# Kernel optimization log

Measured on AMD Instinct MI355X. Metric: run time of the kernel, lower is better.

Reference implementation:

```python
import jax, jax.numpy as jnp
import numpy as np

N = 20000        # nodes
E = 320000       # edges (avg degree 16)
G = 128          # graphs in batch
D_IN = 128
H = 128          # hidden_dim
HEADS = 8
OUT = 2
BN_EPS = 1e-5


def _segment_softmax(logits, seg, num_segments):
    # numerically stable softmax over segments along leading dim
    m = jax.ops.segment_max(logits, seg, num_segments)
    e = jnp.exp(logits - m[seg])
    s = jax.ops.segment_sum(e, seg, num_segments)
    return e / (s[seg] + 1e-16)


def _forward(x, gin1_w1, gin1_b1, gin1_w2, gin1_b2,
             gin2_w1, gin2_b1, gin2_w2, gin2_b2,
             gin3_w1, gin3_b1, gin3_w2, gin3_b2,
             gin4_w1, gin4_b1, gin4_w2, gin4_b2,
             bn1_g, bn1_b, bn2_g, bn2_b, bn3_g, bn3_b, bn4_g, bn4_b, bn5_g, bn5_b,
             gat_w, gat_asrc, gat_adst, gat_bias,
             gate_w, gate_b, fc1_w, fc1_b, fc2_w, fc2_b,
             edge_index, batch):
    src, dst = edge_index[0], edge_index[1]

    def gin(h, w1, b1, w2, b2):
        # GINConv, eps=0: mlp(x + sum_{j->i} x_j)
        agg = jax.ops.segment_sum(h[src], dst, N)
        z = agg + h
        return jax.nn.relu(z @ w1 + b1) @ w2 + b2

    def bn(h, g, b):
        # BatchNorm1d with batch statistics (training-mode normalization)
        mu = h.mean(0)
        var = ((h - mu) ** 2).mean(0)
        return g * (h - mu) * jax.lax.rsqrt(var + BN_EPS) + b

    # dropout is identity at inference
    h = jax.nn.relu(bn(gin(x, gin1_w1, gin1_b1, gin1_w2, gin1_b2), bn1_g, bn1_b))
    h = jax.nn.relu(bn(gin(h, gin2_w1, gin2_b1, gin2_w2, gin2_b2), bn2_g, bn2_b))
    h = jax.nn.relu(bn(gin(h, gin3_w1, gin3_b1, gin3_w2, gin3_b2), bn3_g, bn3_b))
    h = jax.nn.relu(bn(gin(h, gin4_w1, gin4_b1, gin4_w2, gin4_b2), bn4_g, bn4_b))

    # GATConv(2H -> H, heads=HEADS, concat=False) with self-loops (PyG default)
    loop = jnp.arange(N)
    s = jnp.concatenate([src, loop])
    d = jnp.concatenate([dst, loop])
    xh = (h @ gat_w).reshape(N, HEADS, H)                     # [N, heads, H]
    a_s = jnp.einsum('nhc,hc->nh', xh, gat_asrc)              # [N, heads]
    a_d = jnp.einsum('nhc,hc->nh', xh, gat_adst)
    e = jax.nn.leaky_relu(a_s[s] + a_d[d], 0.2)               # [E+N, heads]
    alpha = _segment_softmax(e, d, N)                         # softmax over in-edges of dst
    out = jax.ops.segment_sum(alpha[:, :, None] * xh[s], d, N)  # [N, heads, H]
    h = out.mean(1) + gat_bias                                # concat=False -> mean heads
    h = jax.nn.relu(bn(h, bn5_g, bn5_b))

    # GlobalAttention pooling: softmax(gate_nn(x)) per graph, weighted sum
    gate_logit = (h @ gate_w + gate_b)[:, 0]                  # [N]
    gate = _segment_softmax(gate_logit, batch, G)
    pooled = jax.ops.segment_sum(gate[:, None] * h, batch, G)  # [G, H]

    return jax.nn.relu(pooled @ fc1_w + fc1_b) @ fc2_w + fc2_b  # [G, OUT]


def setup_inputs() -> dict:
    key = jax.random.key(0)
    kit = iter(jax.random.split(key, 64))

    def nrm(shape, s=0.05):
        return jax.random.normal(next(kit), shape, jnp.float32) * s

    inp = {}
    inp['x'] = jax.random.normal(next(kit), (N, D_IN), jnp.float32)
    inp['edge_index'] = jax.random.randint(next(kit), (2, E), 0, N)
    inp['batch'] = jnp.sort(jax.random.randint(next(kit), (N,), 0, G))
    gin_dims = [(D_IN, H), (H, 2 * H), (2 * H, 4 * H), (4 * H, 2 * H)]
    for i, (a, b) in enumerate(gin_dims, 1):
        inp[f'gin{i}_w1'] = nrm((a, b))
        inp[f'gin{i}_b1'] = jnp.zeros((b,), jnp.float32)
        inp[f'gin{i}_w2'] = nrm((b, b))
        inp[f'gin{i}_b2'] = jnp.zeros((b,), jnp.float32)
    for i, dd in enumerate([H, 2 * H, 4 * H, 2 * H, H], 1):
        inp[f'bn{i}_g'] = jnp.ones((dd,), jnp.float32)
        inp[f'bn{i}_b'] = jnp.zeros((dd,), jnp.float32)
    inp['gat_w'] = nrm((2 * H, HEADS * H))
    inp['gat_asrc'] = nrm((HEADS, H))
    inp['gat_adst'] = nrm((HEADS, H))
    inp['gat_bias'] = jnp.zeros((H,), jnp.float32)
    inp['gate_w'] = nrm((H, 1))
    inp['gate_b'] = jnp.zeros((1,), jnp.float32)
    inp['fc1_w'] = nrm((H, 128))
    inp['fc1_b'] = jnp.zeros((128,), jnp.float32)
    inp['fc2_w'] = nrm((128, OUT))
    inp['fc2_b'] = jnp.zeros((OUT,), jnp.float32)
    return inp


def reference(x, edge_index, batch,
              gin1_w1, gin1_b1, gin1_w2, gin1_b2,
              gin2_w1, gin2_b1, gin2_w2, gin2_b2,
              gin3_w1, gin3_b1, gin3_w2, gin3_b2,
              gin4_w1, gin4_b1, gin4_w2, gin4_b2,
              bn1_g, bn1_b, bn2_g, bn2_b, bn3_g, bn3_b, bn4_g, bn4_b, bn5_g, bn5_b,
              gat_w, gat_asrc, gat_adst, gat_bias,
              gate_w, gate_b, fc1_w, fc1_b, fc2_w, fc2_b):
    return _forward(x, gin1_w1, gin1_b1, gin1_w2, gin1_b2,
                    gin2_w1, gin2_b1, gin2_w2, gin2_b2,
                    gin3_w1, gin3_b1, gin3_w2, gin3_b2,
                    gin4_w1, gin4_b1, gin4_w2, gin4_b2,
                    bn1_g, bn1_b, bn2_g, bn2_b, bn3_g, bn3_b, bn4_g, bn4_b, bn5_g, bn5_b,
                    gat_w, gat_asrc, gat_adst, gat_bias,
                    gate_w, gate_b, fc1_w, fc1_b, fc2_w, fc2_b,
                    edge_index, batch)
```

## Files before the change

kernel.cpp:

```cpp
#include <hip/hip_runtime.h>
#include <hip/hip_bf16.h>
#include <math.h>

#define NN 20000
#define NE 320000
#define NG 128

using bf16x8 = __attribute__((ext_vector_type(8))) short;
using f32x4  = __attribute__((ext_vector_type(4))) float;

static __device__ __forceinline__ float lrelu(float v){ return v > 0.f ? v : 0.2f*v; }
static __device__ __forceinline__ float b2f(unsigned short u){ unsigned int v = ((unsigned int)u) << 16; return __uint_as_float(v); }
static __device__ __forceinline__ unsigned short f2b(float f){
  unsigned int x = __float_as_uint(f);
  unsigned int r = x + 0x7fffu + ((x >> 16) & 1u);
  return (unsigned short)(r >> 16);
}
static __device__ __forceinline__ void gl16(const unsigned short* g, unsigned short* l){
  __builtin_amdgcn_global_load_lds((const __attribute__((address_space(1))) void*)g,
                                   (__attribute__((address_space(3))) void*)l, 16, 0, 0);
}
static __device__ __forceinline__ uint4 bn8(uint4 u, const float* scs, const float* shs, int f0){
  float v[8] = { b2f(u.x & 0xffff), b2f(u.x >> 16), b2f(u.y & 0xffff), b2f(u.y >> 16),
                 b2f(u.z & 0xffff), b2f(u.z >> 16), b2f(u.w & 0xffff), b2f(u.w >> 16) };
  #pragma unroll
  for (int j = 0; j < 8; j++) v[j] = fmaxf(v[j]*scs[f0 + j] + shs[f0 + j], 0.f);
  uint4 p;
  p.x = (unsigned int)f2b(v[0]) | ((unsigned int)f2b(v[1]) << 16);
  p.y = (unsigned int)f2b(v[2]) | ((unsigned int)f2b(v[3]) << 16);
  p.z = (unsigned int)f2b(v[4]) | ((unsigned int)f2b(v[5]) << 16);
  p.w = (unsigned int)f2b(v[6]) | ((unsigned int)f2b(v[7]) << 16);
  return p;
}

__global__ void k_hist2(const int* __restrict__ dst, const int* __restrict__ batch,
                        int* __restrict__ deg, int* __restrict__ gdeg){
  int i = blockIdx.x*blockDim.x + threadIdx.x;
  if (i < NE) atomicAdd(&deg[dst[i]], 1);
  else if (i < NE + NN) atomicAdd(&gdeg[batch[i - NE]], 1);
}

__global__ void k_scan2(const int* __restrict__ deg, int* __restrict__ rowptr,
                        const int* __restrict__ gdeg, int* __restrict__ gptr){
  __shared__ int tmp[1024];
  int t = threadIdx.x;
  if (blockIdx.x == 0){
    const int CH = 20;
    int lo = t*CH, hi = min(lo + CH, NN);
    int loc[CH];
    int s = 0;
    for (int i = lo; i < hi; i++){ loc[i - lo] = deg[i]; s += loc[i - lo]; }
    tmp[t] = s; __syncthreads();
    for (int off = 1; off < 1024; off <<= 1){
      int u = (t >= off) ? tmp[t - off] : 0;
      __syncthreads();
      tmp[t] += u;
      __syncthreads();
    }
    int r = tmp[t] - s;
    if (t == 0) rowptr[0] = 0;
    for (int i = lo; i < hi; i++){ r += loc[i - lo]; rowptr[i + 1] = r; }
  } else {
    int v = (t < NG) ? gdeg[t] : 0;
    tmp[t] = v; __syncthreads();
    for (int off = 1; off < 1024; off <<= 1){
      int u = (t >= off) ? tmp[t - off] : 0;
      __syncthreads();
      tmp[t] += u;
      __syncthreads();
    }
    if (t == 0) gptr[0] = 0;
    if (t < NG) gptr[t + 1] = tmp[t];
  }
}

__global__ void k_fill(const int* __restrict__ src, const int* __restrict__ dst,
                       const int* __restrict__ ptr, int* __restrict__ cnt,
                       int* __restrict__ csrc){
  int e = blockIdx.x*blockDim.x + threadIdx.x;
  if (e < NE){
    int d = dst[e];
    int p = atomicAdd(&cnt[d], 1);
    csrc[ptr[d] + p] = src[e];
  }
}

struct WPrep {
  const float* W[9];
  unsigned short* Wt[9];
  int K[9];
  int Nn[9];
  int tileStart[10];
  const float* x;
  unsigned int* xb;
};

__global__ __launch_bounds__(256)
void k_prep2(WPrep P){
  __shared__ float tile[64][65];
  int b = blockIdx.x;
  if (b < P.tileStart[9]){
    int i = 0;
    while (i < 8 && b >= P.tileStart[i+1]) i++;
    int ti = b - P.tileStart[i];
    int K = P.K[i], Nn = P.Nn[i];
    int ntc = Nn >> 6;
    int k0 = (ti / ntc) << 6, n0 = (ti % ntc) << 6;
    int c = threadIdx.x & 63, ro = threadIdx.x >> 6;
    const float* W = P.W[i];
    #pragma unroll
    for (int rr = 0; rr < 16; rr++){
      int r = rr*4 + ro;
      tile[c][r] = W[(size_t)(k0 + r)*Nn + n0 + c];
    }
    __syncthreads();
    unsigned short* Wt = P.Wt[i];
    if (i == 8){
      int hh = n0 >> 7, cl0 = n0 & 127;
      #pragma unroll
      for (int cc = 0; cc < 16; cc++){
        int cidx = cc*4 + ro;
        Wt[(size_t)(cl0 + cidx)*2048 + hh*256 + k0 + c] = f2b(tile[cidx][c]*0.125f);
      }
    } else {
      #pragma unroll
      for (int cc = 0; cc < 16; cc++){
        int cidx = cc*4 + ro;
        Wt[(size_t)(n0 + cidx)*K + k0 + c] = f2b(tile[cidx][c]);
      }
    }
  } else {
    int idx = (b - P.tileStart[9])*256 + threadIdx.x;
    if (idx < NN*64){
      unsigned int lo = f2b(P.x[2*idx]);
      unsigned int hi = f2b(P.x[2*idx + 1]);
      P.xb[idx] = lo | (hi << 16);
    }
  }
}

__global__ void k_wasd(const float* __restrict__ W, const float* __restrict__ asrc,
                       const float* __restrict__ adst, unsigned short* __restrict__ Bt_sc){
  __shared__ float av[128];
  int b = blockIdx.x;
  int h = b & 7, isd = b >> 3;
  int k = threadIdx.x;
  if (k < 128) av[k] = (isd ? adst : asrc)[h*128 + k];
  __syncthreads();
  const float* Wr = W + (size_t)k*1024 + h*128;
  float s = 0.f;
  #pragma unroll 8
  for (int c = 0; c < 128; c++) s += Wr[c]*av[c];
  Bt_sc[b*256 + k] = f2b(s);
}

template<int MODE, int DU>
__global__ __launch_bounds__(256)
void k_agg(const unsigned int* __restrict__ hU, const int* __restrict__ ptr,
           const int* __restrict__ csrc, unsigned int* __restrict__ z,
           const double* __restrict__ stats, const float* __restrict__ g,
           const float* __restrict__ bb, const float* __restrict__ bias){
  const int d = DU*2;
  __shared__ float scs[MODE == 1 ? 512 : 1];
  __shared__ float shs[MODE == 1 ? 512 : 1];
  int t = threadIdx.x;
  if (MODE == 1){
    for (int f = t; f < d; f += 256){
      double inv = 1.0 / (double)NN;
      double mu  = stats[f]*inv;
      double var = stats[d + f]*inv - mu*mu;
      if (var < 0.0) var = 0.0;
      float sc = g[f] * rsqrtf((float)var + 1e-5f);
      scs[f] = sc;
      shs[f] = bb[f] - (float)mu*sc;
    }
    __syncthreads();
  }
  const int npb = 256/DU;
  int n  = blockIdx.x*npb + t/DU;
  int tl = t & (DU - 1);
  int f0 = 2*tl, f1 = f0 + 1;
  float sc0 = 0.f, sh0 = 0.f, sc1 = 0.f, sh1 = 0.f;
  if (MODE == 1){ sc0 = scs[f0]; sh0 = shs[f0]; sc1 = scs[f1]; sh1 = shs[f1]; }
  int beg = ptr[n], deg = ptr[n+1] - beg;
  unsigned int self = hU[(size_t)n*DU + tl];
  float a0, a1;
  if (MODE == 1){
    a0 = fmaxf(b2f(self & 0xffff)*sc0 + sh0, 0.f);
    a1 = fmaxf(b2f(self >> 16)   *sc1 + sh1, 0.f);
  } else {
    a0 = b2f(self & 0xffff);
    a1 = b2f(self >> 16);
  }
  int i = 0;
  for (; i + 8 <= deg; i += 8){
    unsigned int v[8];
    #pragma unroll
    for (int u = 0; u < 8; u++) v[u] = hU[(size_t)csrc[beg + i + u]*DU + tl];
    #pragma unroll
    for (int u = 0; u < 8; u++){
      if (MODE == 1){
        a0 += fmaxf(b2f(v[u] & 0xffff)*sc0 + sh0, 0.f);
        a1 += fmaxf(b2f(v[u] >> 16)   *sc1 + sh1, 0.f);
      } else {
        a0 += b2f(v[u] & 0xffff);
        a1 += b2f(v[u] >> 16);
      }
    }
  }
  for (; i < deg; i++){
    unsigned int v = hU[(size_t)csrc[beg + i]*DU + tl];
    if (MODE == 1){
      a0 += fmaxf(b2f(v & 0xffff)*sc0 + sh0, 0.f);
      a1 += fmaxf(b2f(v >> 16)   *sc1 + sh1, 0.f);
    } else {
      a0 += b2f(v & 0xffff);
      a1 += b2f(v >> 16);
    }
  }
  if (MODE == 2){
    a0 = fmaxf(a0 + bias[f0], 0.f);
    a1 = fmaxf(a1 + bias[f1], 0.f);
  }
  z[(size_t)n*DU + tl] = (unsigned int)f2b(a0) | ((unsigned int)f2b(a1) << 16);
}

template<int ACT, int OBF, int STATS, int PK, int BNA>
__global__ __launch_bounds__(256)
void k_gemm_mfma(const unsigned short* __restrict__ A, const unsigned short* __restrict__ Bt,
                 const float* __restrict__ bias, float* __restrict__ C,
                 unsigned short* __restrict__ Cb, double* __restrict__ stats,
                 const double* __restrict__ bnst, const float* __restrict__ bng,
                 const float* __restrict__ bnb,
                 int M, int Nn, int K){
  const int LDA = BNA ? 40 : 32;
  __shared__ unsigned short As[2][128*(BNA ? 40 : 32)];
  __shared__ unsigned short Bs[2][128*32];
  __shared__ float scs[BNA ? 512 : 1];
  __shared__ float shs[BNA ? 512 : 1];
  const int bm = blockIdx.y*128, bn = blockIdx.x*128;
  const int tid = threadIdx.x;
  const int lane = tid & 63;
  const int wave = tid >> 6;
  const int wm = (wave >> 1)*64, wn = (wave & 1)*64;
  const int lr = lane & 15, lq = lane >> 4;

  f32x4 acc[4][4];
  #pragma unroll
  for (int i = 0; i < 4; i++)
    #pragma unroll
    for (int j = 0; j < 4; j++) acc[i][j] = (f32x4){0.f,0.f,0.f,0.f};

  const int rowA = tid >> 2, q = tid & 3;
  const int ldsOff = wave*16*32;
  const int gmA0 = min(bm + rowA,      M-1);
  const int gmA1 = min(bm + rowA + 64, M-1);
  const unsigned short* pA0 = &A[(size_t)gmA0*K + q*8];
  const unsigned short* pA1 = &A[(size_t)gmA1*K + q*8];
  const unsigned short* pB0 = &Bt[(size_t)(bn + rowA)*K + q*8];
  const unsigned short* pB1 = &Bt[(size_t)(bn + rowA + 64)*K + q*8];

  if (BNA){
    for (int f = tid; f < K; f += 256){
      double inv = 1.0 / (double)NN;
      double mu  = bnst[f]*inv;
      double var = bnst[K + f]*inv - mu*mu;
      if (var < 0.0) var = 0.0;
      float sc = bng[f] * rsqrtf((float)var + 1e-5f);
      scs[f] = sc;
      shs[f] = bnb[f] - (float)mu*sc;
    }
    __syncthreads();
  }

  if (BNA){
    uint4 u0 = *(const uint4*)pA0;
    uint4 u1 = *(const uint4*)pA1;
    int f0 = q*8;
    *(uint4*)&As[0][ rowA      *LDA + q*8] = bn8(u0, scs, shs, f0);
    *(uint4*)&As[0][(rowA + 64)*LDA + q*8] = bn8(u1, scs, shs, f0);
  } else {
    gl16(pA0, &As[0][ldsOff]);
    gl16(pA1, &As[0][ldsOff] + 64*32);
  }
  gl16(pB0, &Bs[0][ldsOff]);
  gl16(pB1, &Bs[0][ldsOff] + 64*32);
  __syncthreads();

  int cur = 0;
  for (int k0 = 0; k0 < K; k0 += 32){
    const int kn = k0 + 32;
    uint4 nu0, nu1;
    if (kn < K){
      if (BNA){
        nu0 = *(const uint4*)(pA0 + kn);
        nu1 = *(const uint4*)(pA1 + kn);
      } else {
        gl16(pA0 + kn, &As[cur^1][ldsOff]);
        gl16(pA1 + kn, &As[cur^1][ldsOff] + 64*32);
      }
      gl16(pB0 + kn, &Bs[cur^1][ldsOff]);
      gl16(pB1 + kn, &Bs[cur^1][ldsOff] + 64*32);
    }
    bf16x8 af[4], bf[4];
    #pragma unroll
    for (int mi = 0; mi < 4; mi++)
      af[mi] = *(const bf16x8*)&As[cur][(wm + mi*16 + lr)*LDA + lq*8];
    #pragma unroll
    for (int ni = 0; ni < 4; ni++)
      bf[ni] = *(const bf16x8*)&Bs[cur][(wn + ni*16 + lr)*32 + lq*8];
    #pragma unroll
    for (int mi = 0; mi < 4; mi++)
      #pragma unroll
      for (int ni = 0; ni < 4; ni++)
        acc[mi][ni] = __builtin_amdgcn_mfma_f32_16x16x32_bf16(af[mi], bf[ni], acc[mi][ni], 0, 0, 0);
    if (BNA && kn < K){
      int f0 = kn + q*8;
      *(uint4*)&As[cur^1][ rowA      *LDA + q*8] = bn8(nu0, scs, shs, f0);
      *(uint4*)&As[cur^1][(rowA + 64)*LDA + q*8] = bn8(nu1, scs, shs, f0);
    }
    __syncthreads();
    cur ^= 1;
  }

  float cs[4] = {0.f,0.f,0.f,0.f}, cq[4] = {0.f,0.f,0.f,0.f};
  #pragma unroll
  for (int mi = 0; mi < 4; mi++){
    #pragma unroll
    for (int j = 0; j < 4; j++){
      int gm = bm + wm + mi*16 + lq*4 + j;
      if (gm < M){
        #pragma unroll
        for (int ni = 0; ni < 4; ni++){
          int gn = bn + wn + ni*16 + lr;
          float v = acc[mi][ni][j] + (bias ? bias[gn] : 0.f);
          if (ACT) v = fmaxf(v, 0.f);
          if (PK){ if (gn < 16) C[(size_t)gm*16 + gn] = v; }
          else if (OBF) Cb[(size_t)gm*Nn + gn] = f2b(v);
          else     C [(size_t)gm*Nn + gn] = v;
          if (STATS){ cs[ni] += v; cq[ni] += v*v; }
        }
      }
    }
  }
  if (STATS){
    #pragma unroll
    for (int ni = 0; ni < 4; ni++){
      float s = cs[ni], qq = cq[ni];
      s += __shfl_xor(s, 16); s += __shfl_xor(s, 32);
      qq += __shfl_xor(qq, 16); qq += __shfl_xor(qq, 32);
      if (lane < 16){
        int gn = bn + wn + ni*16 + lr;
        atomicAdd(&stats[gn],      (double)s);
        atomicAdd(&stats[Nn + gn], (double)qq);
      }
    }
  }
}

__global__ __launch_bounds__(256)
void k_gin1_mlp(const unsigned short* __restrict__ Z, const unsigned short* __restrict__ W1t,
                const float* __restrict__ b1, const unsigned short* __restrict__ W2t,
                const float* __restrict__ b2, unsigned short* __restrict__ Out,
                double* __restrict__ stats, int M){
  __shared__ unsigned short As[2][128*32];
  __shared__ unsigned short Bs[2][128*32];
  __shared__ unsigned short hid[128*136];
  const int bm = blockIdx.x*128;
  const int tid = threadIdx.x;
  const int lane = tid & 63;
  const int wave = tid >> 6;
  const int wm = (wave >> 1)*64, wn = (wave & 1)*64;
  const int lr = lane & 15, lq = lane >> 4;
  const int rowA = tid >> 2, q = tid & 3;
  const int ldsOff = wave*16*32;
  const int gm0 = min(bm + rowA,      M-1);
  const int gm1 = min(bm + rowA + 64, M-1);
  const unsigned short* pA0 = &Z[(size_t)gm0*128 + q*8];
  const unsigned short* pA1 = &Z[(size_t)gm1*128 + q*8];
  const unsigned short* pB0 = &W1t[(size_t)rowA*128 + q*8];
  const unsigned short* pB1 = &W1t[(size_t)(rowA + 64)*128 + q*8];

  f32x4 acc[4][4];
  #pragma unroll
  for (int i = 0; i < 4; i++)
    #pragma unroll
    for (int j = 0; j < 4; j++) acc[i][j] = (f32x4){0.f,0.f,0.f,0.f};

  gl16(pA0, &As[0][ldsOff]);
  gl16(pA1, &As[0][ldsOff] + 64*32);
  gl16(pB0, &Bs[0][ldsOff]);
  gl16(pB1, &Bs[0][ldsOff] + 64*32);
  __syncthreads();
  int cur = 0;
  for (int k0 = 0; k0 < 128; k0 += 32){
    int kn = k0 + 32;
    if (kn < 128){
      gl16(pA0 + kn, &As[cur^1][ldsOff]);
      gl16(pA1 + kn, &As[cur^1][ldsOff] + 64*32);
      gl16(pB0 + kn, &Bs[cur^1][ldsOff]);
      gl16(pB1 + kn, &Bs[cur^1][ldsOff] + 64*32);
    }
    bf16x8 af[4], bf[4];
    #pragma unroll
    for (int mi = 0; mi < 4; mi++)
      af[mi] = *(const bf16x8*)&As[cur][(wm + mi*16 + lr)*32 + lq*8];
    #pragma unroll
    for (int ni = 0; ni < 4; ni++)
      bf[ni] = *(const bf16x8*)&Bs[cur][(wn + ni*16 + lr)*32 + lq*8];
    #pragma unroll
    for (int mi = 0; mi < 4; mi++)
      #pragma unroll
      for (int ni = 0; ni < 4; ni++)
        acc[mi][ni] = __builtin_amdgcn_mfma_f32_16x16x32_bf16(af[mi], bf[ni], acc[mi][ni], 0, 0, 0);
    __syncthreads();
    cur ^= 1;
  }
  {
    float bv[4];
    #pragma unroll
    for (int ni = 0; ni < 4; ni++) bv[ni] = b1[wn + ni*16 + lr];
    #pragma unroll
    for (int mi = 0; mi < 4; mi++)
      #pragma unroll
      for (int j = 0; j < 4; j++){
        int row = wm + mi*16 + lq*4 + j;
        #pragma unroll
        for (int ni = 0; ni < 4; ni++){
          int col = wn + ni*16 + lr;
          hid[row*136 + col] = f2b(fmaxf(acc[mi][ni][j] + bv[ni], 0.f));
        }
      }
  }
  __syncthreads();

  f32x4 acc2[4][4];
  #pragma unroll
  for (int i = 0; i < 4; i++)
    #pragma unroll
    for (int j = 0; j < 4; j++) acc2[i][j] = (f32x4){0.f,0.f,0.f,0.f};
  const unsigned short* pC0 = &W2t[(size_t)rowA*128 + q*8];
  const unsigned short* pC1 = &W2t[(size_t)(rowA + 64)*128 + q*8];
  gl16(pC0, &Bs[0][ldsOff]);
  gl16(pC1, &Bs[0][ldsOff] + 64*32);
  __syncthreads();
  cur = 0;
  for (int k0 = 0; k0 < 128; k0 += 32){
    int kn = k0 + 32;
    if (kn < 128){
      gl16(pC0 + kn, &Bs[cur^1][ldsOff]);
      gl16(pC1 + kn, &Bs[cur^1][ldsOff] + 64*32);
    }
    bf16x8 af[4], bf[4];
    #pragma unroll
    for (int mi = 0; mi < 4; mi++)
      af[mi] = *(const bf16x8*)&hid[(wm + mi*16 + lr)*136 + k0 + lq*8];
    #pragma unroll
    for (int ni = 0; ni < 4; ni++)
      bf[ni] = *(const bf16x8*)&Bs[cur][(wn + ni*16 + lr)*32 + lq*8];
    #pragma unroll
    for (int mi = 0; mi < 4; mi++)
      #pragma unroll
      for (int ni = 0; ni < 4; ni++)
        acc2[mi][ni] = __builtin_amdgcn_mfma_f32_16x16x32_bf16(af[mi], bf[ni], acc2[mi][ni], 0, 0, 0);
    __syncthreads();
    cur ^= 1;
  }
  float cs[4] = {0.f,0.f,0.f,0.f}, cq[4] = {0.f,0.f,0.f,0.f};
  #pragma unroll
  for (int mi = 0; mi < 4; mi++){
    #pragma unroll
    for (int j = 0; j < 4; j++){
      int gm = bm + wm + mi*16 + lq*4 + j;
      if (gm < M){
        #pragma unroll
        for (int ni = 0; ni < 4; ni++){
          int gn = wn + ni*16 + lr;
          float v = acc2[mi][ni][j] + b2[gn];
          Out[(size_t)gm*128 + gn] = f2b(v);
          cs[ni] += v; cq[ni] += v*v;
        }
      }
    }
  }
  #pragma unroll
  for (int ni = 0; ni < 4; ni++){
    float s = cs[ni], qq = cq[ni];
    s += __shfl_xor(s, 16); s += __shfl_xor(s, 32);
    qq += __shfl_xor(qq, 16); qq += __shfl_xor(qq, 32);
    if (lane < 16){
      int gn = wn + ni*16 + lr;
      atomicAdd(&stats[gn],       (double)s);
      atomicAdd(&stats[128 + gn], (double)qq);
    }
  }
}

__global__ __launch_bounds__(256)
void k_gat_agg(const unsigned int* __restrict__ hU, const float* __restrict__ a_sd,
               const int* __restrict__ ptr, const int* __restrict__ csrc,
               const double* __restrict__ st, const float* __restrict__ g,
               const float* __restrict__ bb, unsigned int* __restrict__ agg){
  int n = blockIdx.x, t = threadIdx.x;
  __shared__ float scs[256], shs[256];
  __shared__ float elv[256][9];
  __shared__ int esrc[256];
  __shared__ float red[256];
  __shared__ float ms[8], ssinv[8], adn[8];
  __shared__ float partial[2][8][260];
  {
    int f = t;
    double inv = 1.0/(double)NN;
    double mu = st[f]*inv;
    double var = st[256 + f]*inv - mu*mu;
    if (var < 0.0) var = 0.0;
    float sc = g[f]*rsqrtf((float)var + 1e-5f);
    scs[f] = sc; shs[f] = bb[f] - (float)mu*sc;
  }
  if (t < 8) adn[t] = a_sd[n*16 + 8 + t];
  __syncthreads();
  int beg = ptr[n], deg = ptr[n+1] - beg, tot = deg + 1;
  int head = t >> 5, slot = t & 31;
  int grp = t >> 7, l = t & 127;
  float sc0 = scs[2*l], sh0 = shs[2*l], sc1 = scs[2*l+1], sh1 = shs[2*l+1];
  float acc[16];
  #pragma unroll
  for (int j = 0; j < 16; j++) acc[j] = 0.f;

  if (tot <= 256){
    for (int i = t; i < tot; i += 256) esrc[i] = (i < deg) ? csrc[beg + i] : n;
    __syncthreads();
    for (int i = t; i < tot*8; i += 256){
      int le = i >> 3, hh = i & 7;
      elv[le][hh] = lrelu(a_sd[esrc[le]*16 + hh] + adn[hh]);
    }
    __syncthreads();
    float mx = -1e30f;
    for (int e = slot; e < tot; e += 32) mx = fmaxf(mx, elv[e][head]);
    red[t] = mx; __syncthreads();
    #pragma unroll
    for (int off = 16; off >= 1; off >>= 1){
      if (slot < off) red[t] = fmaxf(red[t], red[t + off]);
      __syncthreads();
    }
    if (slot == 0) ms[head] = red[t];
    __syncthreads();
    float sm = 0.f;
    for (int e = slot; e < tot; e += 32){
      float ex = __expf(elv[e][head] - ms[head]);
      elv[e][head] = ex;
      sm += ex;
    }
    red[t] = sm; __syncthreads();
    #pragma unroll
    for (int off = 16; off >= 1; off >>= 1){
      if (slot < off) red[t] += red[t + off];
      __syncthreads();
    }
    if (slot == 0) ssinv[head] = 1.f / (red[t] + 1e-16f);
    __syncthreads();
    for (int e = grp; e < tot; e += 2){
      unsigned int u = hU[(size_t)esrc[e]*128 + l];
      float v0 = fmaxf(b2f(u & 0xffff)*sc0 + sh0, 0.f);
      float v1 = fmaxf(b2f(u >> 16)   *sc1 + sh1, 0.f);
      #pragma unroll
      for (int h = 0; h < 8; h++){
        float a = elv[e][h];
        acc[2*h]   += a*v0;
        acc[2*h+1] += a*v1;
      }
    }
    __syncthreads();
  } else {
    float mx = -1e30f;
    for (int e = slot; e < tot; e += 32){
      int s = (e < deg) ? csrc[beg + e] : n;
      mx = fmaxf(mx, lrelu(a_sd[s*16 + head] + adn[head]));
    }
    red[t] = mx; __syncthreads();
    #pragma unroll
    for (int off = 16; off >= 1; off >>= 1){
      if (slot < off) red[t] = fmaxf(red[t], red[t + off]);
      __syncthreads();
    }
    if (slot == 0) ms[head] = red[t];
    __syncthreads();
    float sm = 0.f;
    for (int e = slot; e < tot; e += 32){
      int s = (e < deg) ? csrc[beg + e] : n;
      sm += __expf(lrelu(a_sd[s*16 + head] + adn[head]) - ms[head]);
    }
    red[t] = sm; __syncthreads();
    #pragma unroll
    for (int off = 16; off >= 1; off >>= 1){
      if (slot < off) red[t] += red[t + off];
      __syncthreads();
    }
    if (slot == 0) ssinv[head] = 1.f / (red[t] + 1e-16f);
    __syncthreads();
    for (int c0 = 0; c0 < tot; c0 += 256){
      int ce = min(256, tot - c0);
      for (int i = t; i < ce*8; i += 256){
        int le = i >> 3, hh = i & 7;
        int s = (c0 + le < deg) ? csrc[beg + c0 + le] : n;
        if (hh == 0) esrc[le] = s;
        elv[le][hh] = __expf(lrelu(a_sd[s*16 + hh] + adn[hh]) - ms[hh]);
      }
      __syncthreads();
      for (int e = grp; e < ce; e += 2){
        unsigned int u = hU[(size_t)esrc[e]*128 + l];
        float v0 = fmaxf(b2f(u & 0xffff)*sc0 + sh0, 0.f);
        float v1 = fmaxf(b2f(u >> 16)   *sc1 + sh1, 0.f);
        #pragma unroll
        for (int h = 0; h < 8; h++){
          float a = elv[e][h];
          acc[2*h]   += a*v0;
          acc[2*h+1] += a*v1;
        }
      }
      __syncthreads();
    }
  }

  #pragma unroll
  for (int h = 0; h < 8; h++){
    partial[grp][h][2*l]   = acc[2*h];
    partial[grp][h][2*l+1] = acc[2*h+1];
  }
  __syncthreads();
  for (int o = t; o < 1024; o += 256){
    int h = o >> 7, k2 = (o & 127)*2;
    float si = ssinv[h];
    float w0 = (partial[0][h][k2]     + partial[1][h][k2])    *si;
    float w1 = (partial[0][h][k2 + 1] + partial[1][h][k2 + 1])*si;
    agg[(size_t)n*1024 + o] = (unsigned int)f2b(w0) | ((unsigned int)f2b(w1) << 16);
  }
}

__global__ __launch_bounds__(256)
void k_bn_relu_gate(const unsigned short* __restrict__ hpre, unsigned short* __restrict__ hb,
                    int total8, const double* __restrict__ stats,
                    const float* __restrict__ g, const float* __restrict__ b,
                    const float* __restrict__ gatew, const float* __restrict__ gateb,
                    float* __restrict__ logit){
  const int d = 128;
  __shared__ float scs[128], shs[128];
  for (int f = threadIdx.x; f < d; f += blockDim.x){
    double inv = 1.0 / (double)NN;
    double mu  = stats[f]*inv;
    double var = stats[d + f]*inv - mu*mu;
    if (var < 0.0) var = 0.0;
    float sc = g[f] * rsqrtf((float)var + 1e-5f);
    scs[f] = sc;
    shs[f] = b[f] - (float)mu*sc;
  }
  __syncthreads();
  int i = blockIdx.x*blockDim.x + threadIdx.x;
  if (i >= total8) return;
  int i8 = i*8;
  uint4 u = *(const uint4*)&hpre[i8];
  float v[8] = { b2f(u.x & 0xffff), b2f(u.x >> 16), b2f(u.y & 0xffff), b2f(u.y >> 16),
                 b2f(u.z & 0xffff), b2f(u.z >> 16), b2f(u.w & 0xffff), b2f(u.w >> 16) };
  int f0 = i8 & 127;
  float gp = 0.f;
  #pragma unroll
  for (int j = 0; j < 8; j++){
    float y = fmaxf(v[j]*scs[f0 + j] + shs[f0 + j], 0.f);
    v[j] = y;
    gp += y*gatew[f0 + j];
  }
  uint4 p;
  p.x = (unsigned int)f2b(v[0]) | ((unsigned int)f2b(v[1]) << 16);
  p.y = (unsigned int)f2b(v[2]) | ((unsigned int)f2b(v[3]) << 16);
  p.z = (unsigned int)f2b(v[4]) | ((unsigned int)f2b(v[5]) << 16);
  p.w = (unsigned int)f2b(v[6]) | ((unsigned int)f2b(v[7]) << 16);
  *(uint4*)&hb[i8] = p;
  #pragma unroll
  for (int o = 1; o < 16; o <<= 1) gp += __shfl_xor(gp, o);
  if ((threadIdx.x & 15) == 0) logit[i >> 4] = gp + gateb[0];
}

__global__ void k_poolhead(const unsigned short* __restrict__ h, const float* __restrict__ logit,
                           const int* __restrict__ gptr,
                           const float* __restrict__ w1, const float* __restrict__ b1,
                           const float* __restrict__ w2, const float* __restrict__ b2,
                           float* __restrict__ out){
  int g = blockIdx.x, t = threadIdx.x;
  int beg = gptr[g], end = gptr[g+1];
  __shared__ float red[128];
  __shared__ float prow[128];
  __shared__ float r1[128];
  __shared__ float m_sh, s_sh;
  float mx = -1e30f;
  for (int i = beg + t; i < end; i += 128) mx = fmaxf(mx, logit[i]);
  red[t] = mx; __syncthreads();
  for (int off = 64; off > 0; off >>= 1){ if (t < off) red[t] = fmaxf(red[t], red[t + off]); __syncthreads(); }
  if (t == 0) m_sh = red[0];
  __syncthreads();
  float sm = 0.f;
  for (int i = beg + t; i < end; i += 128) sm += __expf(logit[i] - m_sh);
  red[t] = sm; __syncthreads();
  for (int off = 64; off > 0; off >>= 1){ if (t < off) red[t] += red[t + off]; __syncthreads(); }
  if (t == 0) s_sh = red[0] + 1e-16f;
  __syncthreads();
  float acc = 0.f;
  for (int i = beg; i < end; i++){
    float w = __expf(logit[i] - m_sh) / s_sh;
    acc += w * b2f(h[(size_t)i*128 + t]);
  }
  prow[t] = acc;
  __syncthreads();
  float a = b1[t];
  for (int k = 0; k < 128; k++) a += prow[k]*w1[k*128 + t];
  a = fmaxf(a, 0.f);
  red[t] = a*w2[t*2 + 0]; r1[t] = a*w2[t*2 + 1];
  __syncthreads();
  for (int off = 64; off > 0; off >>= 1){
    if (t < off){ red[t] += red[t + off]; r1[t] += r1[t + off]; }
    __syncthreads();
  }
  if (t == 0){ out[g*2 + 0] = red[0] + b2[0]; out[g*2 + 1] = r1[0] + b2[1]; }
}

extern "C" void kernel_launch(void* const* d_in, const int* in_sizes, int n_in,
                              void* d_out, int out_size, void* d_ws, size_t ws_size,
                              hipStream_t stream) {
  const float* x        = (const float*)d_in[0];
  const int*   ei       = (const int*)  d_in[1];
  const int*   batch    = (const int*)  d_in[2];
  const float* gw1[4] = {(const float*)d_in[3],  (const float*)d_in[7],  (const float*)d_in[11], (const float*)d_in[15]};
  const float* gb1[4] = {(const float*)d_in[4],  (const float*)d_in[8],  (const float*)d_in[12], (const float*)d_in[16]};
  const float* gw2[4] = {(const float*)d_in[5],  (const float*)d_in[9],  (const float*)d_in[13], (const float*)d_in[17]};
  const float* gb2[4] = {(const float*)d_in[6],  (const float*)d_in[10], (const float*)d_in[14], (const float*)d_in[18]};
  const float* bng[5] = {(const float*)d_in[19], (const float*)d_in[21], (const float*)d_in[23], (const float*)d_in[25], (const float*)d_in[27]};
  const float* bnb[5] = {(const float*)d_in[20], (const float*)d_in[22], (const float*)d_in[24], (const float*)d_in[26], (const float*)d_in[28]};
  const float* gat_w    = (const float*)d_in[29];
  const float* gat_asrc = (const float*)d_in[30];
  const float* gat_adst = (const float*)d_in[31];
  const float* gat_bias = (const float*)d_in[32];
  const float* gate_w   = (const float*)d_in[33];
  const float* gate_b   = (const float*)d_in[34];
  const float* fc1_w    = (const float*)d_in[35];
  const float* fc1_b    = (const float*)d_in[36];
  const float* fc2_w    = (const float*)d_in[37];
  const float* fc2_b    = (const float*)d_in[38];
  const int* src = ei;
  const int* dst = ei + NE;

  char* wsb = (char*)d_ws;
  size_t off = 0;
  auto take = [&](size_t bytes) -> void* {
    void* p = wsb + off;
    off = (off + bytes + 255) & ~(size_t)255;
    return p;
  };
  unsigned short* hpre  = (unsigned short*)take((size_t)NN*512*2);
  unsigned short* hb    = (unsigned short*)take((size_t)NN*128*2);
  unsigned short* R     = (unsigned short*)take((size_t)NN*2048*2);
  unsigned short* z16   = R;
  unsigned short* hid16 = R + (size_t)NN*512;
  unsigned short* agg16 = R;
  unsigned short* xb    = (unsigned short*)take((size_t)NN*128*2);
  unsigned short* wt    = (unsigned short*)take((size_t)1000000*2);
  int*    deg    = (int*)   take((size_t)NN*4);
  int*    cnt    = (int*)   take((size_t)NN*4);
  int*    gdeg   = (int*)   take((size_t)NG*4);
  double* statsA = (double*)take(2560*8);
  unsigned short* Bt_sc = (unsigned short*)take((size_t)128*256*2);
  float*  a_sd   = (float*) take((size_t)NN*16*4);
  float*  logit  = (float*) take((size_t)NN*4);
  int*    rowptr = (int*)   take((size_t)(NN+1)*4);
  int*    gptr   = (int*)   take((size_t)(NG+1)*4);
  int*    csrc   = (int*)   take((size_t)NE*4);
  (void)ws_size; (void)n_in; (void)in_sizes; (void)out_size;

  unsigned short* wt_g1w1 = wt;
  unsigned short* wt_g1w2 = wt_g1w1 + 128*128;
  unsigned short* wt_g2w1 = wt_g1w2 + 128*128;
  unsigned short* wt_g2w2 = wt_g2w1 + 256*128;
  unsigned short* wt_g3w1 = wt_g2w2 + 256*256;
  unsigned short* wt_g3w2 = wt_g3w1 + 512*256;
  unsigned short* wt_g4w1 = wt_g3w2 + 512*512;
  unsigned short* wt_g4w2 = wt_g4w1 + 256*512;
  unsigned short* wt_gat2 = wt_g4w2 + 256*256;

  double* st1 = statsA + 0;
  double* st2 = statsA + 256;
  double* st3 = statsA + 768;
  double* st4 = statsA + 1792;
  double* st5 = statsA + 2304;

  hipMemsetAsync(deg, 0, (size_t)((char*)(Bt_sc + 128*256) - (char*)deg), stream);

  k_hist2<<<(NE + NN + 255)/256, 256, 0, stream>>>(dst, batch, deg, gdeg);
  k_scan2<<<2, 1024, 0, stream>>>(deg, rowptr, gdeg, gptr);
  k_fill<<<(NE + 255)/256, 256, 0, stream>>>(src, dst, rowptr, cnt, csrc);

  {
    WPrep P;
    const float* Ws[9] = {gw1[0], gw2[0], gw1[1], gw2[1], gw1[2], gw2[2], gw1[3], gw2[3], gat_w};
    unsigned short* Wts[9] = {wt_g1w1, wt_g1w2, wt_g2w1, wt_g2w2, wt_g3w1, wt_g3w2, wt_g4w1, wt_g4w2, wt_gat2};
    int Ks[9]  = {128, 128, 128, 256, 256, 512, 512, 256, 256};
    int Nns[9] = {128, 128, 256, 256, 512, 512, 256, 256, 1024};
    int cum = 0;
    for (int i = 0; i < 9; i++){
      P.W[i] = Ws[i]; P.Wt[i] = Wts[i]; P.K[i] = Ks[i]; P.Nn[i] = Nns[i];
      P.tileStart[i] = cum;
      cum += (Ks[i] >> 6)*(Nns[i] >> 6);
    }
    P.tileStart[9] = cum;
    P.x = x; P.xb = (unsigned int*)xb;
    int xblocks = (NN*64 + 255)/256;
    k_prep2<<<cum + xblocks, 256, 0, stream>>>(P);
  }
  k_wasd<<<16, 256, 0, stream>>>(gat_w, gat_asrc, gat_adst, Bt_sc);

  const int GM = (NN + 127) / 128;
  #define NB3 nullptr, nullptr, nullptr

  k_agg<0,64><<<NN/4, 256, 0, stream>>>((const unsigned int*)xb, rowptr, csrc, (unsigned int*)z16, nullptr, nullptr, nullptr, nullptr);
  k_gin1_mlp<<<GM, 256, 0, stream>>>(z16, wt_g1w1, gb1[0], wt_g1w2, gb2[0], hpre, st1, NN);

  k_agg<1,64><<<NN/4, 256, 0, stream>>>((const unsigned int*)hpre, rowptr, csrc, (unsigned int*)z16, st1, bng[0], bnb[0], nullptr);
  k_gemm_mfma<1,1,0,0,0><<<dim3(2, GM), 256, 0, stream>>>(z16, wt_g2w1, gb1[1], nullptr, hid16, nullptr, NB3, NN, 256, 128);
  k_gemm_mfma<0,1,1,0,0><<<dim3(2, GM), 256, 0, stream>>>(hid16, wt_g2w2, gb2[1], nullptr, hpre, st2, NB3, NN, 256, 256);

  k_agg<1,128><<<NN/2, 256, 0, stream>>>((const unsigned int*)hpre, rowptr, csrc, (unsigned int*)z16, st2, bng[1], bnb[1], nullptr);
  k_gemm_mfma<1,1,0,0,0><<<dim3(4, GM), 256, 0, stream>>>(z16, wt_g3w1, gb1[2], nullptr, hid16, nullptr, NB3, NN, 512, 256);
  k_gemm_mfma<0,1,1,0,0><<<dim3(4, GM), 256, 0, stream>>>(hid16, wt_g3w2, gb2[2], nullptr, hpre, st3, NB3, NN, 512, 512);

  k_gemm_mfma<0,1,0,0,1><<<dim3(2, GM), 256, 0, stream>>>(hpre, wt_g4w1, nullptr, nullptr, hid16, nullptr, st3, bng[2], bnb[2], NN, 256, 512);
  k_agg<2,128><<<NN/2, 256, 0, stream>>>((const unsigned int*)hid16, rowptr, csrc, (unsigned int*)z16, nullptr, nullptr, nullptr, gb1[3]);
  k_gemm_mfma<0,1,1,0,0><<<dim3(2, GM), 256, 0, stream>>>(z16, wt_g4w2, gb2[3], nullptr, hpre, st4, NB3, NN, 256, 256);

  k_gemm_mfma<0,0,0,1,1><<<dim3(1, GM), 256, 0, stream>>>(hpre, Bt_sc, nullptr, a_sd, nullptr, nullptr, st4, bng[3], bnb[3], NN, 128, 256);
  k_gat_agg<<<NN, 256, 0, stream>>>((const unsigned int*)hpre, a_sd, rowptr, csrc, st4, bng[3], bnb[3], (unsigned int*)agg16);
  k_gemm_mfma<0,1,1,0,0><<<dim3(1, GM), 256, 0, stream>>>(agg16, wt_gat2, gat_bias, nullptr, hpre, st5, NB3, NN, 128, 2048);

  k_bn_relu_gate<<<(NN*128/8 + 255)/256, 256, 0, stream>>>(hpre, hb, NN*128/8, st5, bng[4], bnb[4], gate_w, gate_b, logit);
  k_poolhead<<<NG, 128, 0, stream>>>(hb, logit, gptr, fc1_w, fc1_b, fc2_w, fc2_b, (float*)d_out);
}
```

Measured before the change: 617.4 us.

## Rewrite GAT aggregation to one wavefront per node with register softmax

The GAT attention aggregation kernel now assigns one 64-lane wavefront per destination node (four nodes per block) instead of a whole 256-thread block per node. Softmax max and sum are computed in registers with cross-lane shuffles, and attention weights are broadcast by shuffle rather than staged through shared memory. This removes the many __syncthreads barriers, the LDS tree reductions and the final cross-group partial-sum pass. Neighbor features are read as 8-byte vectors per lane. Nodes with more than 64 in-edges take a slower serial tail loop that recomputes the attention weights per edge.

```diff
diff --git a/kernel.cpp b/kernel.cpp
--- a/kernel.cpp
+++ b/kernel.cpp
@@ -497,143 +497,121 @@
 }
 
 __global__ __launch_bounds__(256)
-void k_gat_agg(const unsigned int* __restrict__ hU, const float* __restrict__ a_sd,
-               const int* __restrict__ ptr, const int* __restrict__ csrc,
-               const double* __restrict__ st, const float* __restrict__ g,
-               const float* __restrict__ bb, unsigned int* __restrict__ agg){
-  int n = blockIdx.x, t = threadIdx.x;
-  __shared__ float scs[256], shs[256];
-  __shared__ float elv[256][9];
-  __shared__ int esrc[256];
-  __shared__ float red[256];
-  __shared__ float ms[8], ssinv[8], adn[8];
-  __shared__ float partial[2][8][260];
+void k_gat_agg_w(const unsigned int* __restrict__ hU, const float* __restrict__ a_sd,
+                 const int* __restrict__ ptr, const int* __restrict__ csrc,
+                 const double* __restrict__ st, const float* __restrict__ g,
+                 const float* __restrict__ bb, unsigned int* __restrict__ agg){
+  int wave = threadIdx.x >> 6, lane = threadIdx.x & 63;
+  int n = blockIdx.x*4 + wave;
+  int eslot = lane >> 3, hh = lane & 7;
+  float sc[4], sh[4];
   {
-    int f = t;
     double inv = 1.0/(double)NN;
-    double mu = st[f]*inv;
-    double var = st[256 + f]*inv - mu*mu;
-    if (var < 0.0) var = 0.0;
-    float sc = g[f]*rsqrtf((float)var + 1e-5f);
-    scs[f] = sc; shs[f] = bb[f] - (float)mu*sc;
-  }
-  if (t < 8) adn[t] = a_sd[n*16 + 8 + t];
-  __syncthreads();
+    #pragma unroll
+    for (int j = 0; j < 4; j++){
+      int f = lane*4 + j;
+      double mu = st[f]*inv;
+      double var = st[256 + f]*inv - mu*mu;
+      if (var < 0.0) var = 0.0;
+      float s = g[f]*rsqrtf((float)var + 1e-5f);
+      sc[j] = s; sh[j] = bb[f] - (float)mu*s;
+    }
+  }
+  float adn = a_sd[n*16 + 8 + hh];
   int beg = ptr[n], deg = ptr[n+1] - beg, tot = deg + 1;
-  int head = t >> 5, slot = t & 31;
-  int grp = t >> 7, l = t & 127;
-  float sc0 = scs[2*l], sh0 = shs[2*l], sc1 = scs[2*l+1], sh1 = shs[2*l+1];
-  float acc[16];
-  #pragma unroll
-  for (int j = 0; j < 16; j++) acc[j] = 0.f;
-
-  if (tot <= 256){
-    for (int i = t; i < tot; i += 256) esrc[i] = (i < deg) ? csrc[beg + i] : n;
-    __syncthreads();
-    for (int i = t; i < tot*8; i += 256){
-      int le = i >> 3, hh = i & 7;
-      elv[le][hh] = lrelu(a_sd[esrc[le]*16 + hh] + adn[hh]);
-    }
-    __syncthreads();
-    float mx = -1e30f;
-    for (int e = slot; e < tot; e += 32) mx = fmaxf(mx, elv[e][head]);
-    red[t] = mx; __syncthreads();
-    #pragma unroll
-    for (int off = 16; off >= 1; off >>= 1){
-      if (slot < off) red[t] = fmaxf(red[t], red[t + off]);
-      __syncthreads();
-    }
-    if (slot == 0) ms[head] = red[t];
-    __syncthreads();
-    float sm = 0.f;
-    for (int e = slot; e < tot; e += 32){
-      float ex = __expf(elv[e][head] - ms[head]);
-      elv[e][head] = ex;
-      sm += ex;
-    }
-    red[t] = sm; __syncthreads();
-    #pragma unroll
-    for (int off = 16; off >= 1; off >>= 1){
-      if (slot < off) red[t] += red[t + off];
-      __syncthreads();
-    }
-    if (slot == 0) ssinv[head] = 1.f / (red[t] + 1e-16f);
-    __syncthreads();
-    for (int e = grp; e < tot; e += 2){
-      unsigned int u = hU[(size_t)esrc[e]*128 + l];
-      float v0 = fmaxf(b2f(u & 0xffff)*sc0 + sh0, 0.f);
-      float v1 = fmaxf(b2f(u >> 16)   *sc1 + sh1, 0.f);
+
+  float scb[8];
+  int   sb[8];
+  float m = -1e30f;
+  #pragma unroll
+  for (int c = 0; c < 8; c++){
+    int e = c*8 + eslot;
+    int s_ = (e < deg) ? csrc[beg + e] : n;
+    sb[c] = s_;
+    float v = (e < tot) ? lrelu(a_sd[s_*16 + hh] + adn) : -1e30f;
+    scb[c] = v;
+    m = fmaxf(m, v);
+  }
+  for (int e = 64 + eslot; e < tot; e += 8){
+    int s_ = (e < deg) ? csrc[beg + e] : n;
+    m = fmaxf(m, lrelu(a_sd[s_*16 + hh] + adn));
+  }
+  m = fmaxf(m, __shfl_xor(m, 8));
+  m = fmaxf(m, __shfl_xor(m, 16));
+  m = fmaxf(m, __shfl_xor(m, 32));
+  float S = 0.f;
+  #pragma unroll
+  for (int c = 0; c < 8; c++){
+    float e_ = __expf(scb[c] - m);
+    scb[c] = e_;
+    S += e_;
+  }
+  for (int e = 64 + eslot; e < tot; e += 8){
+    int s_ = (e < deg) ? csrc[beg + e] : n;
+    S += __expf(lrelu(a_sd[s_*16 + hh] + adn) - m);
+  }
+  S += __shfl_xor(S, 8); S += __shfl_xor(S, 16); S += __shfl_xor(S, 32);
+  float rinv = 1.f / (S + 1e-16f);
+  #pragma unroll
+  for (int c = 0; c < 8; c++) scb[c] *= rinv;
+
+  float acc[8][4];
+  #pragma unroll
+  for (int h = 0; h < 8; h++)
+    #pragma unroll
+    for (int j = 0; j < 4; j++) acc[h][j] = 0.f;
+
+  #pragma unroll
+  for (int c = 0; c < 8; c++){
+    int ebase = c*8;
+    if (ebase >= tot) break;
+    int   sbc  = sb[c];
+    float scbc = scb[c];
+    #pragma unroll
+    for (int ee = 0; ee < 8; ee++){
+      int e = ebase + ee;
+      if (e >= tot) break;
+      int sl = ee*8;
+      int srcN = __shfl(sbc, sl);
+      float al[8];
+      #pragma unroll
+      for (int h = 0; h < 8; h++) al[h] = __shfl(scbc, sl + h);
+      uint2 u = *(const uint2*)&hU[(size_t)srcN*128 + lane*2];
+      float v0 = fmaxf(b2f(u.x & 0xffff)*sc[0] + sh[0], 0.f);
+      float v1 = fmaxf(b2f(u.x >> 16)   *sc[1] + sh[1], 0.f);
+      float v2 = fmaxf(b2f(u.y & 0xffff)*sc[2] + sh[2], 0.f);
+      float v3 = fmaxf(b2f(u.y >> 16)   *sc[3] + sh[3], 0.f);
       #pragma unroll
       for (int h = 0; h < 8; h++){
-        float a = elv[e][h];
-        acc[2*h]   += a*v0;
-        acc[2*h+1] += a*v1;
+        acc[h][0] += al[h]*v0; acc[h][1] += al[h]*v1;
+        acc[h][2] += al[h]*v2; acc[h][3] += al[h]*v3;
       }
     }
-    __syncthreads();
-  } else {
-    float mx = -1e30f;
-    for (int e = slot; e < tot; e += 32){
-      int s = (e < deg) ? csrc[beg + e] : n;
-      mx = fmaxf(mx, lrelu(a_sd[s*16 + head] + adn[head]));
-    }
-    red[t] = mx; __syncthreads();
-    #pragma unroll
-    for (int off = 16; off >= 1; off >>= 1){
-      if (slot < off) red[t] = fmaxf(red[t], red[t + off]);
-      __syncthreads();
-    }
-    if (slot == 0) ms[head] = red[t];
-    __syncthreads();
-    float sm = 0.f;
-    for (int e = slot; e < tot; e += 32){
-      int s = (e < deg) ? csrc[beg + e] : n;
-      sm += __expf(lrelu(a_sd[s*16 + head] + adn[head]) - ms[head]);
-    }
-    red[t] = sm; __syncthreads();
-    #pragma unroll
-    for (int off = 16; off >= 1; off >>= 1){
-      if (slot < off) red[t] += red[t + off];
-      __syncthreads();
-    }
-    if (slot == 0) ssinv[head] = 1.f / (red[t] + 1e-16f);
-    __syncthreads();
-    for (int c0 = 0; c0 < tot; c0 += 256){
-      int ce = min(256, tot - c0);
-      for (int i = t; i < ce*8; i += 256){
-        int le = i >> 3, hh = i & 7;
-        int s = (c0 + le < deg) ? csrc[beg + c0 + le] : n;
-        if (hh == 0) esrc[le] = s;
-        elv[le][hh] = __expf(lrelu(a_sd[s*16 + hh] + adn[hh]) - ms[hh]);
-      }
-      __syncthreads();
-      for (int e = grp; e < ce; e += 2){
-        unsigned int u = hU[(size_t)esrc[e]*128 + l];
-        float v0 = fmaxf(b2f(u & 0xffff)*sc0 + sh0, 0.f);
-        float v1 = fmaxf(b2f(u >> 16)   *sc1 + sh1, 0.f);
-        #pragma unroll
-        for (int h = 0; h < 8; h++){
-          float a = elv[e][h];
-          acc[2*h]   += a*v0;
-          acc[2*h+1] += a*v1;
-        }
-      }
-      __syncthreads();
+  }
+  for (int e = 64; e < tot; e++){
+    int s_ = (e < deg) ? csrc[beg + e] : n;
+    float a = __expf(lrelu(a_sd[s_*16 + hh] + adn) - m)*rinv;
+    float al[8];
+    #pragma unroll
+    for (int h = 0; h < 8; h++) al[h] = __shfl(a, h);
+    uint2 u = *(const uint2*)&hU[(size_t)s_*128 + lane*2];
+    float v0 = fmaxf(b2f(u.x & 0xffff)*sc[0] + sh[0], 0.f);
+    float v1 = fmaxf(b2f(u.x >> 16)   *sc[1] + sh[1], 0.f);
+    float v2 = fmaxf(b2f(u.y & 0xffff)*sc[2] + sh[2], 0.f);
+    float v3 = fmaxf(b2f(u.y >> 16)   *sc[3] + sh[3], 0.f);
+    #pragma unroll
+    for (int h = 0; h < 8; h++){
+      acc[h][0] += al[h]*v0; acc[h][1] += al[h]*v1;
+      acc[h][2] += al[h]*v2; acc[h][3] += al[h]*v3;
     }
   }
 
   #pragma unroll
   for (int h = 0; h < 8; h++){
-    partial[grp][h][2*l]   = acc[2*h];
-    partial[grp][h][2*l+1] = acc[2*h+1];
-  }
-  __syncthreads();
-  for (int o = t; o < 1024; o += 256){
-    int h = o >> 7, k2 = (o & 127)*2;
-    float si = ssinv[h];
-    float w0 = (partial[0][h][k2]     + partial[1][h][k2])    *si;
-    float w1 = (partial[0][h][k2 + 1] + partial[1][h][k2 + 1])*si;
-    agg[(size_t)n*1024 + o] = (unsigned int)f2b(w0) | ((unsigned int)f2b(w1) << 16);
+    uint2 o;
+    o.x = (unsigned int)f2b(acc[h][0]) | ((unsigned int)f2b(acc[h][1]) << 16);
+    o.y = (unsigned int)f2b(acc[h][2]) | ((unsigned int)f2b(acc[h][3]) << 16);
+    *(uint2*)&agg[(size_t)n*1024 + h*128 + lane*2] = o;
   }
 }
 
@@ -834,7 +812,7 @@
   k_gemm_mfma<0,1,1,0,0><<<dim3(2, GM), 256, 0, stream>>>(z16, wt_g4w2, gb2[3], nullptr, hpre, st4, NB3, NN, 256, 256);
 
   k_gemm_mfma<0,0,0,1,1><<<dim3(1, GM), 256, 0, stream>>>(hpre, Bt_sc, nullptr, a_sd, nullptr, nullptr, st4, bng[3], bnb[3], NN, 128, 256);
-  k_gat_agg<<<NN, 256, 0, stream>>>((const unsigned int*)hpre, a_sd, rowptr, csrc, st4, bng[3], bnb[3], (unsigned int*)agg16);
+  k_gat_agg_w<<<NN/4, 256, 0, stream>>>((const unsigned int*)hpre, a_sd, rowptr, csrc, st4, bng[3], bnb[3], (unsigned int*)agg16);
   k_gemm_mfma<0,1,1,0,0><<<dim3(1, GM), 256, 0, stream>>>(agg16, wt_gat2, gat_bias, nullptr, hpre, st5, NB3, NN, 128, 2048);
 
   k_bn_relu_gate<<<(NN*128/8 + 255)/256, 256, 0, stream>>>(hpre, hb, NN*128/8, st5, bng[4], bnb[4], gate_w, gate_b, logit);
```

After: 571.8 us. 1.08x faster.
